# Performance work log

Measured on AMD Instinct MI355X. Metric: run time of the kernel, lower is better.

## Reference

```python
import jax, jax.numpy as jnp
import numpy as np
from jax import lax

HID, PROJ, DYN = 256, 256, 64
HW, BS, NQ = 6400, 16, 100


def setup_inputs() -> dict:
    key = jax.random.key(0)
    ks = jax.random.split(key, 10)
    p = lambda k, shape: jax.random.normal(k, shape, jnp.float32) * 0.02
    return {
        "query_feat": jax.random.normal(ks[0], (HW, BS, HID), jnp.float32),
        "support_feat": jax.random.normal(ks[1], (NQ, BS, HID), jnp.float32),
        "h": 80,
        "w": 80,
        "Wq": p(ks[2], (HID, PROJ)), "bq": jnp.zeros((PROJ,), jnp.float32),
        "Ws": p(ks[3], (HID, PROJ)), "bsp": jnp.zeros((PROJ,), jnp.float32),
        "W1": p(ks[4], (PROJ, DYN)), "b1": jnp.zeros((DYN,), jnp.float32),
        "W2": p(ks[5], (DYN, HID)), "b2": jnp.zeros((HID,), jnp.float32),
    }


def reference(query_feat, support_feat, h, w, Wq, bq, Ws, bsp, W1, b1, W2, b2):
    # query_feat: [hw, bs, c] -> [bs, hw, c]; support_feat: [nq, bs, c] -> [bs, nq, c]
    qf = jnp.transpose(query_feat, (1, 0, 2))
    sf = jnp.transpose(support_feat, (1, 0, 2))
    bsz, nq = sf.shape[0], sf.shape[1]
    hw = h * w

    fs_proj = sf @ Ws + bsp                      # [bs, nq, proj]
    fq_proj = qf @ Wq + bq                       # [bs, hw, proj]
    pattern = jnp.tanh(jax.nn.relu(fs_proj @ W1 + b1) @ W2 + b2)
    fs_feat = (pattern + 1.0) * fs_proj          # [bs, nq, proj]

    # bmm(fq, fs^T).T -> [bs, nq, hw]
    sim = jnp.einsum("bkp,bnp->bnk", fq_proj, fs_feat)
    similarity = sim.reshape(bsz, nq, h, w)

    # coordinate grid: x varies along w, y along h; flattened [hw, 2]
    gy = jnp.arange(h, dtype=jnp.float32) + 0.5
    gx = jnp.arange(w, dtype=jnp.float32) + 0.5
    X, Y = jnp.meshgrid(gx, gy, indexing="xy")  # each [h, w]
    coord = jnp.stack([X, Y], axis=-1).reshape(hw, 2)
    side = jnp.array([w, h], dtype=jnp.float32)

    sm = jax.nn.softmax(sim, axis=-1)            # [bs, nq, hw]
    proposal_for_loss = jnp.einsum("bnk,kd->bnd", sm, coord) / side

    # argmax peak -> one-hot -> 3x3 max-pool dilation (note (w,h) reshape per original)
    max_pos = jnp.argmax(sim, axis=-1)           # [bs, nq]
    max_mask = jax.nn.one_hot(max_pos, hw, dtype=jnp.float32).reshape(bsz, nq, w, h)
    local_mask = lax.reduce_window(
        max_mask, -jnp.inf, lax.max,
        window_dimensions=(1, 1, 3, 3), window_strides=(1, 1, 1, 1),
        padding=[(0, 0), (0, 0), (1, 1), (1, 1)],
    ).reshape(bsz, nq, hw)

    local_sm = sm * local_mask
    local_sm = local_sm / (jnp.sum(local_sm, axis=-1, keepdims=True) + 1e-10)
    proposals = jnp.einsum("bnk,kd->bnd", local_sm, coord) / side

    return proposal_for_loss, similarity, proposals
```

## Files before the change

### kernel.cpp

```cpp
#include <hip/hip_runtime.h>

#define HID 256
#define PROJ 256
#define DYN 64
#define HWD 6400
#define BSZ 16
#define NQ 100
#define HH 80
#define WW 80

typedef unsigned short u16;
typedef u16 u16x8 __attribute__((ext_vector_type(8)));
typedef __bf16 bf16x8 __attribute__((ext_vector_type(8)));
typedef float f32x4 __attribute__((ext_vector_type(4)));

__device__ __forceinline__ float bf2f(u16 h) {
    union { unsigned u; float f; } c; c.u = ((unsigned)h) << 16; return c.f;
}
__device__ __forceinline__ u16 f2bf(float f) {
    union { float f; unsigned u; } c; c.f = f;
    return (u16)((c.u + 0x7FFFu + ((c.u >> 16) & 1u)) >> 16);
}

__global__ __launch_bounds__(256) void kpre(
    const float* __restrict__ support,
    const float* __restrict__ Wq, const float* __restrict__ bq,
    const float* __restrict__ Ws, const float* __restrict__ bsp,
    const float* __restrict__ W1, const float* __restrict__ b1,
    const float* __restrict__ W2, const float* __restrict__ b2,
    u16* __restrict__ pack, float* __restrict__ cvec)
{
    const int c = blockIdx.x;
    const int b = blockIdx.y;
    const int t = threadIdx.x;
    const int wv = t >> 6, lane = t & 63;

    __shared__ __align__(16) float sf_t[HID][8];
    __shared__ __align__(16) float fsp[8][PROJ];
    __shared__ __align__(16) float hid[8][DYN];
    __shared__ __align__(16) float fsf_t[PROJ][8];
    __shared__ float cacc[8][4];

    {
        const int nl = t >> 5;
        const int i0 = (t & 31) * 8;
        const int n = c * 8 + nl;
        float v[8];
        if (n < NQ) {
            const float* sp = support + (size_t)n * (BSZ * HID) + (size_t)b * HID + i0;
            const f32x4 a = *reinterpret_cast<const f32x4*>(sp);
            const f32x4 bb = *reinterpret_cast<const f32x4*>(sp + 4);
            v[0]=a[0]; v[1]=a[1]; v[2]=a[2]; v[3]=a[3];
            v[4]=bb[0]; v[5]=bb[1]; v[6]=bb[2]; v[7]=bb[3];
        } else {
            #pragma unroll
            for (int j = 0; j < 8; ++j) v[j] = 0.f;
        }
        #pragma unroll
        for (int j = 0; j < 8; ++j) sf_t[i0 + j][nl] = v[j];
    }
    __syncthreads();

    {
        const int p = t;
        float acc[8];
        #pragma unroll
        for (int n = 0; n < 8; ++n) acc[n] = 0.f;
        for (int i = 0; i < HID; ++i) {
            const float w = Ws[(size_t)i * PROJ + p];
            const f32x4 s0 = *reinterpret_cast<const f32x4*>(&sf_t[i][0]);
            const f32x4 s1 = *reinterpret_cast<const f32x4*>(&sf_t[i][4]);
            acc[0] += s0[0] * w; acc[1] += s0[1] * w;
            acc[2] += s0[2] * w; acc[3] += s0[3] * w;
            acc[4] += s1[0] * w; acc[5] += s1[1] * w;
            acc[6] += s1[2] * w; acc[7] += s1[3] * w;
        }
        const float bb = bsp[p];
        #pragma unroll
        for (int n = 0; n < 8; ++n) fsp[n][p] = acc[n] + bb;
    }
    __syncthreads();

    {
        const int d = lane;
        #pragma unroll
        for (int pass = 0; pass < 2; ++pass) {
            const int nl = pass * 4 + wv;
            float a = 0.f;
            for (int p2 = 0; p2 < PROJ; ++p2)
                a += fsp[nl][p2] * W1[(size_t)p2 * DYN + d];
            a += b1[d];
            hid[nl][d] = a > 0.f ? a : 0.f;
        }
    }
    __syncthreads();

    float cp[8];
    {
        const int p = t;
        const float bqv = bq[p];
        const float b2v = b2[p];
        #pragma unroll
        for (int nl = 0; nl < 8; ++nl) {
            float a = 0.f;
            for (int d = 0; d < DYN; ++d)
                a += hid[nl][d] * W2[(size_t)d * PROJ + p];
            const float pat = tanhf(a + b2v);
            const float ff = (pat + 1.f) * fsp[nl][p];
            fsf_t[p][nl] = ff;
            cp[nl] = bqv * ff;
        }
    }
    __syncthreads();

    #pragma unroll
    for (int nl = 0; nl < 8; ++nl) {
        float v = cp[nl];
        for (int off = 32; off > 0; off >>= 1) v += __shfl_down(v, off);
        if (lane == 0) cacc[nl][wv] = v;
    }
    __syncthreads();
    if (t < 8) {
        const int n = c * 8 + t;
        if (n < NQ) cvec[b * NQ + n] = cacc[t][0] + cacc[t][1] + cacc[t][2] + cacc[t][3];
    }

    {
        const int h = t;
        float acc[8];
        #pragma unroll
        for (int n = 0; n < 8; ++n) acc[n] = 0.f;
        for (int p0 = 0; p0 < PROJ; p0 += 8) {
            const float* wp = Wq + (size_t)h * PROJ + p0;
            const f32x4 w0 = *reinterpret_cast<const f32x4*>(wp);
            const f32x4 w1 = *reinterpret_cast<const f32x4*>(wp + 4);
            float wv8[8] = {w0[0], w0[1], w0[2], w0[3], w1[0], w1[1], w1[2], w1[3]};
            #pragma unroll
            for (int j = 0; j < 8; ++j) {
                const float w = wv8[j];
                const f32x4 f0 = *reinterpret_cast<const f32x4*>(&fsf_t[p0 + j][0]);
                const f32x4 f1 = *reinterpret_cast<const f32x4*>(&fsf_t[p0 + j][4]);
                acc[0] += f0[0] * w; acc[1] += f0[1] * w;
                acc[2] += f0[2] * w; acc[3] += f0[3] * w;
                acc[4] += f1[0] * w; acc[5] += f1[1] * w;
                acc[6] += f1[2] * w; acc[7] += f1[3] * w;
            }
        }
        const int ks = h >> 5, quad = (h >> 3) & 3, j = h & 7;
        const int nt = c >> 1;
        #pragma unroll
        for (int nl = 0; nl < 8; ++nl) {
            const int n = c * 8 + nl;
            const float f = (n < NQ) ? acc[nl] : 0.f;
            const u16 hi = f2bf(f);
            const u16 lo = f2bf(f - bf2f(hi));
            const int nit = (c & 1) * 8 + nl;
            const int lane2 = quad * 16 + nit;
            const size_t base = ((((size_t)b * 2 + 0) * 8 + ks) * 8 + nt) * 512 + lane2 * 8 + j;
            const size_t baseL = base + (size_t)8 * 8 * 512;
            pack[base] = hi;
            pack[baseL] = lo;
        }
    }
}

__global__ __launch_bounds__(256) void ksim(
    const float* __restrict__ qf,
    const u16* __restrict__ pack,
    const float* __restrict__ cvec,
    float* __restrict__ sim)
{
    const int mc = blockIdx.x;
    const int b  = blockIdx.y;
    const int wv = threadIdx.x >> 6;
    const int lane = threadIdx.x & 63;
    const int quad = lane >> 4, l16 = lane & 15;

    f32x4 acc[7];
    #pragma unroll
    for (int nt = 0; nt < 7; ++nt) acc[nt] = (f32x4){0.f, 0.f, 0.f, 0.f};

    const int row = mc * 64 + wv * 16 + l16;
    const float* ap = qf + (size_t)row * (BSZ * HID) + b * HID + quad * 8;
    const u16* pb = pack + (size_t)b * (2 * 8 * 8 * 64 * 8) + (size_t)lane * 8;

    #pragma unroll 2
    for (int ks = 0; ks < 8; ++ks) {
        bf16x8 ahi, alo;
        {
            const float* fp = ap + ks * 32;
            const f32x4 v0 = *reinterpret_cast<const f32x4*>(fp);
            const f32x4 v1 = *reinterpret_cast<const f32x4*>(fp + 4);
            float v[8] = {v0[0], v0[1], v0[2], v0[3], v1[0], v1[1], v1[2], v1[3]};
            #pragma unroll
            for (int j = 0; j < 8; ++j) {
                const __bf16 h = (__bf16)v[j];
                ahi[j] = h;
                alo[j] = (__bf16)(v[j] - (float)h);
            }
        }
        #pragma unroll
        for (int nt = 0; nt < 7; ++nt) {
            u16x8 uh = *reinterpret_cast<const u16x8*>(pb + ((size_t)(0 * 8 + ks) * 8 + nt) * 512);
            u16x8 ul = *reinterpret_cast<const u16x8*>(pb + ((size_t)(1 * 8 + ks) * 8 + nt) * 512);
            const bf16x8 bh = __builtin_bit_cast(bf16x8, uh);
            const bf16x8 bl = __builtin_bit_cast(bf16x8, ul);
            acc[nt] = __builtin_amdgcn_mfma_f32_16x16x32_bf16(ahi, bh, acc[nt], 0, 0, 0);
            acc[nt] = __builtin_amdgcn_mfma_f32_16x16x32_bf16(ahi, bl, acc[nt], 0, 0, 0);
            acc[nt] = __builtin_amdgcn_mfma_f32_16x16x32_bf16(alo, bh, acc[nt], 0, 0, 0);
        }
    }

    const int kbase = mc * 64 + wv * 16 + quad * 4;
    #pragma unroll
    for (int nt = 0; nt < 7; ++nt) {
        const int n = nt * 16 + l16;
        if (n >= NQ) continue;
        const float cadd = cvec[b * NQ + n];
        f32x4 o = acc[nt];
        o[0] += cadd; o[1] += cadd; o[2] += cadd; o[3] += cadd;
        *reinterpret_cast<f32x4*>(sim + (size_t)(b * NQ + n) * HWD + kbase) = o;
    }
}

__global__ __launch_bounds__(256) void kfin(
    const float* __restrict__ sim,
    float* __restrict__ out)
{
    const int bn = blockIdx.x;
    const int t = threadIdx.x;

    __shared__ __align__(16) float row[HWD];
    __shared__ float redA[256];
    __shared__ float redB[256];
    __shared__ float redC[256];
    __shared__ int   redi[256];
    __shared__ float smax_s;
    __shared__ int   samax_s;

    const float* src = sim + (size_t)bn * HWD;

    for (int i4 = t; i4 < HWD / 4; i4 += 256)
        reinterpret_cast<f32x4*>(row)[i4] = reinterpret_cast<const f32x4*>(src)[i4];
    __syncthreads();

    float bv = -3.4e38f; int bi = 0;
    for (int i = t; i < HWD; i += 256) {
        const float v = row[i];
        if (v > bv) { bv = v; bi = i; }
    }
    redA[t] = bv; redi[t] = bi;
    __syncthreads();
    for (int s = 128; s > 0; s >>= 1) {
        if (t < s) {
            const float v2 = redA[t + s]; const int i2 = redi[t + s];
            if (v2 > redA[t] || (v2 == redA[t] && i2 < redi[t])) { redA[t] = v2; redi[t] = i2; }
        }
        __syncthreads();
    }
    if (t == 0) { smax_s = redA[0]; samax_s = redi[0]; }
    __syncthreads();
    const float mx = smax_s;

    float s1 = 0.f, sx = 0.f, sy = 0.f;
    for (int i = t; i < HWD; i += 256) {
        const float e = __expf(row[i] - mx);
        row[i] = e;
        s1 += e;
        sx += e * ((float)(i % WW) + 0.5f);
        sy += e * ((float)(i / WW) + 0.5f);
    }
    redA[t] = s1; redB[t] = sx; redC[t] = sy;
    __syncthreads();
    for (int s = 128; s > 0; s >>= 1) {
        if (t < s) { redA[t] += redA[t + s]; redB[t] += redB[t + s]; redC[t] += redC[t + s]; }
        __syncthreads();
    }

    if (t == 0) {
        const float S = redA[0], WX = redB[0], WY = redC[0];
        const int am = samax_s;
        const int r = am / WW, ccol = am % WW;
        float lsum = 0.f, lx = 0.f, ly = 0.f;
        for (int dy = -1; dy <= 1; ++dy) {
            const int yy = r + dy;
            if (yy < 0 || yy >= HH) continue;
            for (int dx = -1; dx <= 1; ++dx) {
                const int xx = ccol + dx;
                if (xx < 0 || xx >= WW) continue;
                const float e = row[yy * WW + xx];
                lsum += e; lx += e * ((float)xx + 0.5f); ly += e * ((float)yy + 0.5f);
            }
        }
        const float invS = 1.f / S;
        out[(size_t)bn * 2 + 0] = WX * invS / (float)WW;
        out[(size_t)bn * 2 + 1] = WY * invS / (float)HH;
        const float den = lsum + 1e-10f * S;
        const size_t pbase = 3200 + (size_t)BSZ * NQ * HWD;
        out[pbase + (size_t)bn * 2 + 0] = lx / den / (float)WW;
        out[pbase + (size_t)bn * 2 + 1] = ly / den / (float)HH;
    }
}

extern "C" void kernel_launch(void* const* d_in, const int* in_sizes, int n_in,
                              void* d_out, int out_size, void* d_ws, size_t ws_size,
                              hipStream_t stream) {
    const float* qf  = (const float*)d_in[0];
    const float* sf  = (const float*)d_in[1];
    const float* Wq  = (const float*)d_in[4];
    const float* bq  = (const float*)d_in[5];
    const float* Ws  = (const float*)d_in[6];
    const float* bsp = (const float*)d_in[7];
    const float* W1  = (const float*)d_in[8];
    const float* b1  = (const float*)d_in[9];
    const float* W2  = (const float*)d_in[10];
    const float* b2  = (const float*)d_in[11];

    u16*   pack  = (u16*)d_ws;
    float* cvec  = (float*)((char*)d_ws + 2097152);
    float* out   = (float*)d_out;
    float* sim   = out + 3200;

    kpre<<<dim3(16, 16), 256, 0, stream>>>(sf, Wq, bq, Ws, bsp, W1, b1, W2, b2, pack, cvec);
    ksim<<<dim3(100, 16), 256, 0, stream>>>(qf, pack, cvec, sim);
    kfin<<<1600, 256, 0, stream>>>(sim, out);
}
```

Before: 310.0 us.

## Double M-tile per wave in ksim with A prefetch; wave-per-row finalize kernel

The similarity GEMM now gives each wave two 16-row M tiles, so every B fragment loaded from the pack buffer is reused twice. It also prefetches the next k-slice of query activations while the MFMAs for the current slice run, and the grid is halved to match. The finalize kernel drops the shared-memory, block-wide reductions and assigns one wavefront per (b,n) row: it reads the row twice from global memory and uses shuffle reductions for the argmax and for the softmax-weighted sums, including the 3x3 local window. The trade-offs are higher register pressure in ksim and a second global read of each sim row in kfin instead of a cached copy in LDS.

After: 297.5 us. 4.0% less time.

```diff
diff --git a/kernel.cpp b/kernel.cpp
--- a/kernel.cpp
+++ b/kernel.cpp
@@ -176,50 +176,86 @@
     const int lane = threadIdx.x & 63;
     const int quad = lane >> 4, l16 = lane & 15;
 
-    f32x4 acc[7];
-    #pragma unroll
-    for (int nt = 0; nt < 7; ++nt) acc[nt] = (f32x4){0.f, 0.f, 0.f, 0.f};
-
-    const int row = mc * 64 + wv * 16 + l16;
-    const float* ap = qf + (size_t)row * (BSZ * HID) + b * HID + quad * 8;
+    f32x4 acc[2][7];
+    #pragma unroll
+    for (int mt = 0; mt < 2; ++mt)
+        #pragma unroll
+        for (int nt = 0; nt < 7; ++nt) acc[mt][nt] = (f32x4){0.f, 0.f, 0.f, 0.f};
+
+    const float* ap[2];
+    #pragma unroll
+    for (int mt = 0; mt < 2; ++mt) {
+        const int row = mc * 128 + wv * 32 + mt * 16 + l16;
+        ap[mt] = qf + (size_t)row * (BSZ * HID) + b * HID + quad * 8;
+    }
     const u16* pb = pack + (size_t)b * (2 * 8 * 8 * 64 * 8) + (size_t)lane * 8;
 
-    #pragma unroll 2
+    f32x4 af[2][2], afn[2][2];
+    #pragma unroll
+    for (int mt = 0; mt < 2; ++mt) {
+        af[mt][0] = *reinterpret_cast<const f32x4*>(ap[mt] + 0);
+        af[mt][1] = *reinterpret_cast<const f32x4*>(ap[mt] + 4);
+    }
+
+    #pragma unroll
     for (int ks = 0; ks < 8; ++ks) {
-        bf16x8 ahi, alo;
-        {
-            const float* fp = ap + ks * 32;
-            const f32x4 v0 = *reinterpret_cast<const f32x4*>(fp);
-            const f32x4 v1 = *reinterpret_cast<const f32x4*>(fp + 4);
-            float v[8] = {v0[0], v0[1], v0[2], v0[3], v1[0], v1[1], v1[2], v1[3]};
-            #pragma unroll
-            for (int j = 0; j < 8; ++j) {
-                const __bf16 h = (__bf16)v[j];
-                ahi[j] = h;
-                alo[j] = (__bf16)(v[j] - (float)h);
+        u16x8 uh[7], ul[7];
+        #pragma unroll
+        for (int nt = 0; nt < 7; ++nt) {
+            uh[nt] = *reinterpret_cast<const u16x8*>(pb + ((size_t)(0 * 8 + ks) * 8 + nt) * 512);
+            ul[nt] = *reinterpret_cast<const u16x8*>(pb + ((size_t)(1 * 8 + ks) * 8 + nt) * 512);
+        }
+        if (ks < 7) {
+            #pragma unroll
+            for (int mt = 0; mt < 2; ++mt) {
+                afn[mt][0] = *reinterpret_cast<const f32x4*>(ap[mt] + (ks + 1) * 32 + 0);
+                afn[mt][1] = *reinterpret_cast<const f32x4*>(ap[mt] + (ks + 1) * 32 + 4);
             }
         }
+        bf16x8 ahi[2], alo[2];
+        #pragma unroll
+        for (int mt = 0; mt < 2; ++mt) {
+            #pragma unroll
+            for (int half = 0; half < 2; ++half) {
+                #pragma unroll
+                for (int j = 0; j < 4; ++j) {
+                    const float v = af[mt][half][j];
+                    const __bf16 h = (__bf16)v;
+                    ahi[mt][half * 4 + j] = h;
+                    alo[mt][half * 4 + j] = (__bf16)(v - (float)h);
+                }
+            }
+        }
         #pragma unroll
         for (int nt = 0; nt < 7; ++nt) {
-            u16x8 uh = *reinterpret_cast<const u16x8*>(pb + ((size_t)(0 * 8 + ks) * 8 + nt) * 512);
-            u16x8 ul = *reinterpret_cast<const u16x8*>(pb + ((size_t)(1 * 8 + ks) * 8 + nt) * 512);
-            const bf16x8 bh = __builtin_bit_cast(bf16x8, uh);
-            const bf16x8 bl = __builtin_bit_cast(bf16x8, ul);
-            acc[nt] = __builtin_amdgcn_mfma_f32_16x16x32_bf16(ahi, bh, acc[nt], 0, 0, 0);
-            acc[nt] = __builtin_amdgcn_mfma_f32_16x16x32_bf16(ahi, bl, acc[nt], 0, 0, 0);
-            acc[nt] = __builtin_amdgcn_mfma_f32_16x16x32_bf16(alo, bh, acc[nt], 0, 0, 0);
-        }
-    }
-
-    const int kbase = mc * 64 + wv * 16 + quad * 4;
-    #pragma unroll
-    for (int nt = 0; nt < 7; ++nt) {
-        const int n = nt * 16 + l16;
-        if (n >= NQ) continue;
-        const float cadd = cvec[b * NQ + n];
-        f32x4 o = acc[nt];
-        o[0] += cadd; o[1] += cadd; o[2] += cadd; o[3] += cadd;
-        *reinterpret_cast<f32x4*>(sim + (size_t)(b * NQ + n) * HWD + kbase) = o;
+            const bf16x8 bh = __builtin_bit_cast(bf16x8, uh[nt]);
+            const bf16x8 bl = __builtin_bit_cast(bf16x8, ul[nt]);
+            #pragma unroll
+            for (int mt = 0; mt < 2; ++mt) {
+                acc[mt][nt] = __builtin_amdgcn_mfma_f32_16x16x32_bf16(ahi[mt], bh, acc[mt][nt], 0, 0, 0);
+                acc[mt][nt] = __builtin_amdgcn_mfma_f32_16x16x32_bf16(ahi[mt], bl, acc[mt][nt], 0, 0, 0);
+                acc[mt][nt] = __builtin_amdgcn_mfma_f32_16x16x32_bf16(alo[mt], bh, acc[mt][nt], 0, 0, 0);
+            }
+        }
+        #pragma unroll
+        for (int mt = 0; mt < 2; ++mt) {
+            af[mt][0] = afn[mt][0];
+            af[mt][1] = afn[mt][1];
+        }
+    }
+
+    #pragma unroll
+    for (int mt = 0; mt < 2; ++mt) {
+        const int kbase = mc * 128 + wv * 32 + mt * 16 + quad * 4;
+        #pragma unroll
+        for (int nt = 0; nt < 7; ++nt) {
+            const int n = nt * 16 + l16;
+            if (n >= NQ) continue;
+            const float cadd = cvec[b * NQ + n];
+            f32x4 o = acc[mt][nt];
+            o[0] += cadd; o[1] += cadd; o[2] += cadd; o[3] += cadd;
+            *reinterpret_cast<f32x4*>(sim + (size_t)(b * NQ + n) * HWD + kbase) = o;
+        }
     }
 }
 
@@ -227,78 +263,68 @@
     const float* __restrict__ sim,
     float* __restrict__ out)
 {
-    const int bn = blockIdx.x;
-    const int t = threadIdx.x;
-
-    __shared__ __align__(16) float row[HWD];
-    __shared__ float redA[256];
-    __shared__ float redB[256];
-    __shared__ float redC[256];
-    __shared__ int   redi[256];
-    __shared__ float smax_s;
-    __shared__ int   samax_s;
-
+    const int wv = threadIdx.x >> 6;
+    const int lane = threadIdx.x & 63;
+    const int bn = blockIdx.x * 4 + wv;
     const float* src = sim + (size_t)bn * HWD;
 
-    for (int i4 = t; i4 < HWD / 4; i4 += 256)
-        reinterpret_cast<f32x4*>(row)[i4] = reinterpret_cast<const f32x4*>(src)[i4];
-    __syncthreads();
-
     float bv = -3.4e38f; int bi = 0;
-    for (int i = t; i < HWD; i += 256) {
-        const float v = row[i];
-        if (v > bv) { bv = v; bi = i; }
-    }
-    redA[t] = bv; redi[t] = bi;
-    __syncthreads();
-    for (int s = 128; s > 0; s >>= 1) {
-        if (t < s) {
-            const float v2 = redA[t + s]; const int i2 = redi[t + s];
-            if (v2 > redA[t] || (v2 == redA[t] && i2 < redi[t])) { redA[t] = v2; redi[t] = i2; }
-        }
-        __syncthreads();
-    }
-    if (t == 0) { smax_s = redA[0]; samax_s = redi[0]; }
-    __syncthreads();
-    const float mx = smax_s;
+    #pragma unroll
+    for (int j = 0; j < 25; ++j) {
+        const f32x4 v = *reinterpret_cast<const f32x4*>(src + j * 256 + lane * 4);
+        #pragma unroll
+        for (int k = 0; k < 4; ++k) {
+            if (v[k] > bv) { bv = v[k]; bi = j * 256 + lane * 4 + k; }
+        }
+    }
+    #pragma unroll
+    for (int m = 1; m < 64; m <<= 1) {
+        const float ov = __shfl_xor(bv, m);
+        const int oi = __shfl_xor(bi, m);
+        if (ov > bv || (ov == bv && oi < bi)) { bv = ov; bi = oi; }
+    }
+    const int xc = bi % WW, yc = bi / WW;
 
     float s1 = 0.f, sx = 0.f, sy = 0.f;
-    for (int i = t; i < HWD; i += 256) {
-        const float e = __expf(row[i] - mx);
-        row[i] = e;
-        s1 += e;
-        sx += e * ((float)(i % WW) + 0.5f);
-        sy += e * ((float)(i / WW) + 0.5f);
-    }
-    redA[t] = s1; redB[t] = sx; redC[t] = sy;
-    __syncthreads();
-    for (int s = 128; s > 0; s >>= 1) {
-        if (t < s) { redA[t] += redA[t + s]; redB[t] += redB[t + s]; redC[t] += redC[t + s]; }
-        __syncthreads();
-    }
-
-    if (t == 0) {
-        const float S = redA[0], WX = redB[0], WY = redC[0];
-        const int am = samax_s;
-        const int r = am / WW, ccol = am % WW;
-        float lsum = 0.f, lx = 0.f, ly = 0.f;
-        for (int dy = -1; dy <= 1; ++dy) {
-            const int yy = r + dy;
-            if (yy < 0 || yy >= HH) continue;
-            for (int dx = -1; dx <= 1; ++dx) {
-                const int xx = ccol + dx;
-                if (xx < 0 || xx >= WW) continue;
-                const float e = row[yy * WW + xx];
-                lsum += e; lx += e * ((float)xx + 0.5f); ly += e * ((float)yy + 0.5f);
-            }
-        }
-        const float invS = 1.f / S;
-        out[(size_t)bn * 2 + 0] = WX * invS / (float)WW;
-        out[(size_t)bn * 2 + 1] = WY * invS / (float)HH;
-        const float den = lsum + 1e-10f * S;
+    float wl = 0.f, wx = 0.f, wyv = 0.f;
+    int x = (lane * 4) % WW, y = (lane * 4) / WW;
+    #pragma unroll
+    for (int j = 0; j < 25; ++j) {
+        const f32x4 v = *reinterpret_cast<const f32x4*>(src + j * 256 + lane * 4);
+        #pragma unroll
+        for (int k = 0; k < 4; ++k) {
+            int xe = x + k, ye = y;
+            if (xe >= WW) { xe -= WW; ye += 1; }
+            const float e = __expf(v[k] - bv);
+            const float fx = (float)xe + 0.5f;
+            const float fy = (float)ye + 0.5f;
+            s1 += e; sx += e * fx; sy += e * fy;
+            const int dx = xe - xc, dy = ye - yc;
+            const bool inw = (dx >= -1 && dx <= 1 && dy >= -1 && dy <= 1);
+            const float ew = inw ? e : 0.f;
+            wl += ew; wx += ew * fx; wyv += ew * fy;
+        }
+        x += 16; y += 3;
+        if (x >= WW) { x -= WW; y += 1; }
+    }
+    #pragma unroll
+    for (int m = 1; m < 64; m <<= 1) {
+        s1 += __shfl_xor(s1, m);
+        sx += __shfl_xor(sx, m);
+        sy += __shfl_xor(sy, m);
+        wl += __shfl_xor(wl, m);
+        wx += __shfl_xor(wx, m);
+        wyv += __shfl_xor(wyv, m);
+    }
+
+    if (lane == 0) {
+        const float invS = 1.f / s1;
+        out[(size_t)bn * 2 + 0] = sx * invS / (float)WW;
+        out[(size_t)bn * 2 + 1] = sy * invS / (float)HH;
+        const float den = wl + 1e-10f * s1;
         const size_t pbase = 3200 + (size_t)BSZ * NQ * HWD;
-        out[pbase + (size_t)bn * 2 + 0] = lx / den / (float)WW;
-        out[pbase + (size_t)bn * 2 + 1] = ly / den / (float)HH;
+        out[pbase + (size_t)bn * 2 + 0] = wx / den / (float)WW;
+        out[pbase + (size_t)bn * 2 + 1] = wyv / den / (float)HH;
     }
 }
 
@@ -322,6 +348,6 @@
     float* sim   = out + 3200;
 
     kpre<<<dim3(16, 16), 256, 0, stream>>>(sf, Wq, bq, Ws, bsp, W1, b1, W2, b2, pack, cvec);
-    ksim<<<dim3(100, 16), 256, 0, stream>>>(qf, pack, cvec, sim);
-    kfin<<<1600, 256, 0, stream>>>(sim, out);
-}
+    ksim<<<dim3(50, 16), 256, 0, stream>>>(qf, pack, cvec, sim);
+    kfin<<<400, 256, 0, stream>>>(sim, out);
+}
```
